# Kernel tuning notes

Hardware: AMD Instinct MI355X
Metric: run time of the kernel (lower is better)

## Reference

```python
import jax, jax.numpy as jnp
import numpy as np

B, S, IN = 1, 50000, 128
N = B * S
E = 800000
HID, HEADS, OUT = 64, 2, 64
NEG_SLOPE = 0.2
BN_EPS = 1e-5


def setup_inputs() -> dict:
    key = jax.random.key(0)
    ks = jax.random.split(key, 12)
    s = 0.1
    return {
        "data": jax.random.normal(ks[0], (B, S, IN), jnp.float32),
        "edge_index": jax.random.randint(ks[1], (2, E), 0, N, dtype=jnp.int64),
        "W0": jax.random.normal(ks[2], (IN, HEADS * HID), jnp.float32) * s,
        "att_src0": jax.random.normal(ks[3], (HEADS, HID), jnp.float32) * s,
        "att_dst0": jax.random.normal(ks[4], (HEADS, HID), jnp.float32) * s,
        "bias0": jnp.zeros((HEADS * HID,), jnp.float32),
        "gamma0": jnp.ones((HEADS * HID,), jnp.float32),
        "beta0": jnp.zeros((HEADS * HID,), jnp.float32),
        "W1": jax.random.normal(ks[5], (HEADS * HID, OUT), jnp.float32) * s,
        "att_src1": jax.random.normal(ks[6], (1, OUT), jnp.float32) * s,
        "att_dst1": jax.random.normal(ks[7], (1, OUT), jnp.float32) * s,
        "bias1": jnp.zeros((OUT,), jnp.float32),
    }


def gat_conv(x, edge_index, W, att_src, att_dst, bias, heads, ch, concat):
    n = x.shape[0]
    loop = jnp.arange(n, dtype=edge_index.dtype)
    src = jnp.concatenate([edge_index[0], loop])  # PyG adds self-loops by default
    dst = jnp.concatenate([edge_index[1], loop])
    h = (x @ W).reshape(n, heads, ch)  # [N,H,C]
    a_src = (h * att_src).sum(-1)  # [N,H]
    a_dst = (h * att_dst).sum(-1)  # [N,H]
    e = jax.nn.leaky_relu(a_src[src] + a_dst[dst], NEG_SLOPE)  # [Etot,H]
    m = jax.ops.segment_max(e, dst, num_segments=n)  # segment softmax over dst
    ex = jnp.exp(e - m[dst])
    denom = jax.ops.segment_sum(ex, dst, num_segments=n)
    alpha = ex / (denom[dst] + 1e-16)  # [Etot,H]
    out = jax.ops.segment_sum(h[src] * alpha[:, :, None], dst, num_segments=n)  # [N,H,C]
    out = out.reshape(n, heads * ch) if concat else out.mean(axis=1)
    return out + bias


def reference(data, edge_index, W0, att_src0, att_dst0, bias0, gamma0, beta0,
              W1, att_src1, att_dst1, bias1):
    x = data.reshape(N, IN)
    x = gat_conv(x, edge_index, W0, att_src0, att_dst0, bias0, HEADS, HID, True)
    mu = x.mean(axis=0)
    var = x.var(axis=0)
    x = (x - mu) * jax.lax.rsqrt(var + BN_EPS) * gamma0 + beta0  # BatchNorm1d (batch stats)
    x = jax.nn.elu(x)
    x = gat_conv(x, edge_index, W1, att_src1, att_dst1, bias1, 1, OUT, False)
    return x.reshape(B, S, OUT)
```

## Files before the change

kernel.cpp:

```cpp
#include <hip/hip_runtime.h>
#include <hip/hip_fp16.h>
#include <math.h>

#define N_NODES 50000
#define E_EDGES 800000
#define NEG_SLOPE 0.2f
#define BN_EPS 1e-5f
#define SCAN_NBLK ((N_NODES + 1023) / 1024)

__device__ __forceinline__ float lrelu(float v) { return v > 0.f ? v : NEG_SLOPE * v; }

__global__ void k_zero(int* __restrict__ counts, float* __restrict__ bn_sum,
                       float* __restrict__ bn_sumsq) {
  int i = blockIdx.x * 256 + threadIdx.x;
  if (i < N_NODES + 1) counts[i] = 0;
  if (i < 128) { bn_sum[i] = 0.f; bn_sumsq[i] = 0.f; }
}

__global__ void k_hist(const int* __restrict__ dst, int* __restrict__ counts) {
  int e = blockIdx.x * 256 + threadIdx.x;
  if (e < E_EDGES) atomicAdd(&counts[dst[e]], 1);
}

__global__ __launch_bounds__(256) void k_scan1(const int* __restrict__ counts,
                                               int* __restrict__ tmp_scan,
                                               int* __restrict__ blk_sums) {
  __shared__ int ts[256];
  int t = threadIdx.x;
  int base = blockIdx.x * 1024 + t * 4;
  int c0 = (base + 0 < N_NODES) ? counts[base + 0] : 0;
  int c1 = (base + 1 < N_NODES) ? counts[base + 1] : 0;
  int c2 = (base + 2 < N_NODES) ? counts[base + 2] : 0;
  int c3 = (base + 3 < N_NODES) ? counts[base + 3] : 0;
  int s = c0 + c1 + c2 + c3;
  ts[t] = s;
  __syncthreads();
  for (int off = 1; off < 256; off <<= 1) {
    int v = (t >= off) ? ts[t - off] : 0;
    __syncthreads();
    ts[t] += v;
    __syncthreads();
  }
  int excl = ts[t] - s;
  if (t == 255) blk_sums[blockIdx.x] = ts[255];
  if (base + 0 < N_NODES) tmp_scan[base + 0] = excl;
  if (base + 1 < N_NODES) tmp_scan[base + 1] = excl + c0;
  if (base + 2 < N_NODES) tmp_scan[base + 2] = excl + c0 + c1;
  if (base + 3 < N_NODES) tmp_scan[base + 3] = excl + c0 + c1 + c2;
}

__global__ void k_scan2(int* __restrict__ blk_sums) {
  int t = threadIdx.x;
  int orig = (t < SCAN_NBLK) ? blk_sums[t] : 0;
  int v = orig;
#pragma unroll
  for (int off = 1; off < 64; off <<= 1) {
    int u = __shfl_up(v, off);
    if (t >= off) v += u;
  }
  if (t < SCAN_NBLK) blk_sums[t] = v - orig;
}

__global__ __launch_bounds__(256) void k_scan3(const int* __restrict__ tmp_scan,
                                               const int* __restrict__ blk_sums,
                                               int* __restrict__ row_ptr,
                                               int* __restrict__ cursor) {
  int i = blockIdx.x * 256 + threadIdx.x;
  if (i < N_NODES) {
    int v = tmp_scan[i] + blk_sums[i >> 10];
    row_ptr[i] = v;
    cursor[i] = v;
  }
  if (i == 0) row_ptr[N_NODES] = E_EDGES;
}

__global__ void k_scatter(const int* __restrict__ src, const int* __restrict__ dst,
                          int* __restrict__ cursor, int* __restrict__ csr_src) {
  int e = blockIdx.x * 256 + threadIdx.x;
  if (e < E_EDGES) {
    int d = dst[e];
    int pos = atomicAdd(&cursor[d], 1);
    csr_src[pos] = src[e];
  }
}

__global__ __launch_bounds__(256) void k_gemm0(
    const float* __restrict__ x, const float* __restrict__ W,
    const float* __restrict__ att_s, const float* __restrict__ att_d,
    __half* __restrict__ h, float* __restrict__ a_src, float* __restrict__ a_dst) {
  __shared__ float xs[64 * 132];
  int t = threadIdx.x;
  int rowBase = blockIdx.x * 64;
#pragma unroll
  for (int j = 0; j < 8; j++) {
    int id = t + 256 * j;
    int row = id >> 5;
    int kk = (id & 31) * 4;
    float4 v = make_float4(0.f, 0.f, 0.f, 0.f);
    int gr = rowBase + row;
    if (gr < N_NODES) v = *(const float4*)&x[(size_t)gr * 128 + kk];
    *(float4*)&xs[row * 132 + kk] = v;
  }
  __syncthreads();

  int tc = t & 31, tr = t >> 5;
  int c = tc * 4, r0 = tr * 8;
  float acc[8][4];
#pragma unroll
  for (int i = 0; i < 8; i++)
#pragma unroll
    for (int j = 0; j < 4; j++) acc[i][j] = 0.f;

  for (int k4 = 0; k4 < 128; k4 += 4) {
    float4 wv[4];
#pragma unroll
    for (int kk = 0; kk < 4; kk++) wv[kk] = *(const float4*)&W[(k4 + kk) * 128 + c];
    float4 xv[8];
#pragma unroll
    for (int i = 0; i < 8; i++) xv[i] = *(const float4*)&xs[(r0 + i) * 132 + k4];
#pragma unroll
    for (int i = 0; i < 8; i++) {
      acc[i][0] += xv[i].x * wv[0].x + xv[i].y * wv[1].x + xv[i].z * wv[2].x + xv[i].w * wv[3].x;
      acc[i][1] += xv[i].x * wv[0].y + xv[i].y * wv[1].y + xv[i].z * wv[2].y + xv[i].w * wv[3].y;
      acc[i][2] += xv[i].x * wv[0].z + xv[i].y * wv[1].z + xv[i].z * wv[2].z + xv[i].w * wv[3].z;
      acc[i][3] += xv[i].x * wv[0].w + xv[i].y * wv[1].w + xv[i].z * wv[2].w + xv[i].w * wv[3].w;
    }
  }

  float as4[4], ad4[4];
#pragma unroll
  for (int j = 0; j < 4; j++) { as4[j] = att_s[c + j]; ad4[j] = att_d[c + j]; }
  int head = tc >> 4;
#pragma unroll
  for (int i = 0; i < 8; i++) {
    int gr = rowBase + r0 + i;
    float ps = acc[i][0] * as4[0] + acc[i][1] * as4[1] + acc[i][2] * as4[2] + acc[i][3] * as4[3];
    float pd = acc[i][0] * ad4[0] + acc[i][1] * ad4[1] + acc[i][2] * ad4[2] + acc[i][3] * ad4[3];
#pragma unroll
    for (int msk = 1; msk <= 8; msk <<= 1) {
      ps += __shfl_xor(ps, msk);
      pd += __shfl_xor(pd, msk);
    }
    if (gr < N_NODES) {
      __half2 p01 = __floats2half2_rn(acc[i][0], acc[i][1]);
      __half2 p23 = __floats2half2_rn(acc[i][2], acc[i][3]);
      uint2 pk;
      pk.x = *(unsigned int*)&p01;
      pk.y = *(unsigned int*)&p23;
      *(uint2*)&h[(size_t)gr * 128 + c] = pk;
      if ((t & 15) == 0) {
        a_src[gr * 2 + head] = ps;
        a_dst[gr * 2 + head] = pd;
      }
    }
  }
}

__global__ __launch_bounds__(256) void k_agg0(
    const int* __restrict__ row_ptr, const int* __restrict__ csr_src,
    const __half* __restrict__ h, const float* __restrict__ a_src,
    const float* __restrict__ a_dst, const float* __restrict__ bias,
    float* __restrict__ out) {
  int node = (blockIdx.x * blockDim.x + threadIdx.x) >> 6;
  if (node >= N_NODES) return;
  int l = threadIdx.x & 63;
  int head = l >> 5;
  int c = l * 2;
  float ad = a_dst[node * 2 + head];
  float m = lrelu(a_src[node * 2 + head] + ad);
  float d = 1.f;
  __half2 hvp = *(const __half2*)&h[(size_t)node * 128 + c];
  float2 hv = __half22float2(hvp);
  float acc0 = hv.x, acc1 = hv.y;
  int beg = row_ptr[node], end = row_ptr[node + 1];
  int i = beg;
  for (; i + 4 <= end; i += 4) {
    int s0 = csr_src[i], s1 = csr_src[i + 1], s2 = csr_src[i + 2], s3 = csr_src[i + 3];
    float e0 = lrelu(a_src[s0 * 2 + head] + ad);
    float e1 = lrelu(a_src[s1 * 2 + head] + ad);
    float e2 = lrelu(a_src[s2 * 2 + head] + ad);
    float e3 = lrelu(a_src[s3 * 2 + head] + ad);
    __half2 p0 = *(const __half2*)&h[(size_t)s0 * 128 + c];
    __half2 p1 = *(const __half2*)&h[(size_t)s1 * 128 + c];
    __half2 p2 = *(const __half2*)&h[(size_t)s2 * 128 + c];
    __half2 p3 = *(const __half2*)&h[(size_t)s3 * 128 + c];
    float nm = fmaxf(fmaxf(m, e0), fmaxf(fmaxf(e1, e2), e3));
    float sc = __expf(m - nm);
    float w0 = __expf(e0 - nm), w1 = __expf(e1 - nm);
    float w2 = __expf(e2 - nm), w3 = __expf(e3 - nm);
    d = d * sc + (w0 + w1) + (w2 + w3);
    float2 f0 = __half22float2(p0), f1 = __half22float2(p1);
    float2 f2 = __half22float2(p2), f3 = __half22float2(p3);
    acc0 = acc0 * sc + w0 * f0.x + w1 * f1.x + w2 * f2.x + w3 * f3.x;
    acc1 = acc1 * sc + w0 * f0.y + w1 * f1.y + w2 * f2.y + w3 * f3.y;
    m = nm;
  }
  for (; i < end; i++) {
    int s = csr_src[i];
    float ee = lrelu(a_src[s * 2 + head] + ad);
    __half2 pp = *(const __half2*)&h[(size_t)s * 128 + c];
    float nm = fmaxf(m, ee);
    float sc = __expf(m - nm);
    float w = __expf(ee - nm);
    float2 ff = __half22float2(pp);
    d = d * sc + w;
    acc0 = acc0 * sc + w * ff.x;
    acc1 = acc1 * sc + w * ff.y;
    m = nm;
  }
  float inv = 1.f / d;
  float2 o;
  o.x = acc0 * inv + bias[c];
  o.y = acc1 * inv + bias[c + 1];
  *(float2*)&out[(size_t)node * 128 + c] = o;
}

__global__ __launch_bounds__(256) void k_bnstats(const float* __restrict__ x,
                                                 float* __restrict__ bn_sum,
                                                 float* __restrict__ bn_sumsq) {
  int f = threadIdx.x & 127;
  int half = threadIdx.x >> 7;
  float s = 0.f, s2 = 0.f;
  for (int r = blockIdx.x * 2 + half; r < N_NODES; r += gridDim.x * 2) {
    float v = x[(size_t)r * 128 + f];
    s += v;
    s2 += v * v;
  }
  __shared__ float ls[256], ls2[256];
  ls[threadIdx.x] = s;
  ls2[threadIdx.x] = s2;
  __syncthreads();
  if (half == 0) {
    atomicAdd(&bn_sum[f], s + ls[f + 128]);
    atomicAdd(&bn_sumsq[f], s2 + ls2[f + 128]);
  }
}

__global__ void k_bnfinal(const float* __restrict__ sum, const float* __restrict__ sumsq,
                          const float* __restrict__ gamma, const float* __restrict__ beta,
                          float* __restrict__ scale, float* __restrict__ shift) {
  int f = threadIdx.x;
  float mu = sum[f] / (float)N_NODES;
  float var = sumsq[f] / (float)N_NODES - mu * mu;
  float sc = gamma[f] * rsqrtf(var + BN_EPS);
  scale[f] = sc;
  shift[f] = beta[f] - mu * sc;
}

__global__ __launch_bounds__(256) void k_gemm1(
    const float* __restrict__ x, const float* __restrict__ W,
    const float* __restrict__ scale, const float* __restrict__ shift,
    const float* __restrict__ att_s, const float* __restrict__ att_d,
    __half* __restrict__ h, float* __restrict__ a_src, float* __restrict__ a_dst) {
  __shared__ float xs[64 * 132];
  int t = threadIdx.x;
  int rowBase = blockIdx.x * 64;
#pragma unroll
  for (int j = 0; j < 8; j++) {
    int id = t + 256 * j;
    int row = id >> 5;
    int kk = (id & 31) * 4;
    float4 v = make_float4(0.f, 0.f, 0.f, 0.f);
    int gr = rowBase + row;
    if (gr < N_NODES) {
      float4 raw = *(const float4*)&x[(size_t)gr * 128 + kk];
      float4 sc = *(const float4*)&scale[kk];
      float4 sh = *(const float4*)&shift[kk];
      v.x = raw.x * sc.x + sh.x;
      v.y = raw.y * sc.y + sh.y;
      v.z = raw.z * sc.z + sh.z;
      v.w = raw.w * sc.w + sh.w;
      v.x = v.x > 0.f ? v.x : __expf(v.x) - 1.f;
      v.y = v.y > 0.f ? v.y : __expf(v.y) - 1.f;
      v.z = v.z > 0.f ? v.z : __expf(v.z) - 1.f;
      v.w = v.w > 0.f ? v.w : __expf(v.w) - 1.f;
    }
    *(float4*)&xs[row * 132 + kk] = v;
  }
  __syncthreads();

  int tc = t & 15, tr = t >> 4;
  int c = tc * 4, r0 = tr * 4;
  float acc[4][4];
#pragma unroll
  for (int i = 0; i < 4; i++)
#pragma unroll
    for (int j = 0; j < 4; j++) acc[i][j] = 0.f;

  for (int k4 = 0; k4 < 128; k4 += 4) {
    float4 wv[4];
#pragma unroll
    for (int kk = 0; kk < 4; kk++) wv[kk] = *(const float4*)&W[(k4 + kk) * 64 + c];
    float4 xv[4];
#pragma unroll
    for (int i = 0; i < 4; i++) xv[i] = *(const float4*)&xs[(r0 + i) * 132 + k4];
#pragma unroll
    for (int i = 0; i < 4; i++) {
      acc[i][0] += xv[i].x * wv[0].x + xv[i].y * wv[1].x + xv[i].z * wv[2].x + xv[i].w * wv[3].x;
      acc[i][1] += xv[i].x * wv[0].y + xv[i].y * wv[1].y + xv[i].z * wv[2].y + xv[i].w * wv[3].y;
      acc[i][2] += xv[i].x * wv[0].z + xv[i].y * wv[1].z + xv[i].z * wv[2].z + xv[i].w * wv[3].z;
      acc[i][3] += xv[i].x * wv[0].w + xv[i].y * wv[1].w + xv[i].z * wv[2].w + xv[i].w * wv[3].w;
    }
  }

  float as4[4], ad4[4];
#pragma unroll
  for (int j = 0; j < 4; j++) { as4[j] = att_s[c + j]; ad4[j] = att_d[c + j]; }
#pragma unroll
  for (int i = 0; i < 4; i++) {
    int gr = rowBase + r0 + i;
    float ps = acc[i][0] * as4[0] + acc[i][1] * as4[1] + acc[i][2] * as4[2] + acc[i][3] * as4[3];
    float pd = acc[i][0] * ad4[0] + acc[i][1] * ad4[1] + acc[i][2] * ad4[2] + acc[i][3] * ad4[3];
#pragma unroll
    for (int msk = 1; msk <= 8; msk <<= 1) {
      ps += __shfl_xor(ps, msk);
      pd += __shfl_xor(pd, msk);
    }
    if (gr < N_NODES) {
      __half2 p01 = __floats2half2_rn(acc[i][0], acc[i][1]);
      __half2 p23 = __floats2half2_rn(acc[i][2], acc[i][3]);
      uint2 pk;
      pk.x = *(unsigned int*)&p01;
      pk.y = *(unsigned int*)&p23;
      *(uint2*)&h[(size_t)gr * 64 + c] = pk;
      if ((t & 15) == 0) {
        a_src[gr] = ps;
        a_dst[gr] = pd;
      }
    }
  }
}

__global__ __launch_bounds__(256) void k_agg1(
    const int* __restrict__ row_ptr, const int* __restrict__ csr_src,
    const __half* __restrict__ h, const float* __restrict__ a_src,
    const float* __restrict__ a_dst, const float* __restrict__ bias,
    float* __restrict__ out) {
  int node = (blockIdx.x * blockDim.x + threadIdx.x) >> 6;
  if (node >= N_NODES) return;
  int l = threadIdx.x & 63;
  float ad = a_dst[node];
  float m = lrelu(a_src[node] + ad);
  float d = 1.f;
  float acc = __half2float(h[(size_t)node * 64 + l]);
  int beg = row_ptr[node], end = row_ptr[node + 1];
  int i = beg;
  for (; i + 4 <= end; i += 4) {
    int s0 = csr_src[i], s1 = csr_src[i + 1], s2 = csr_src[i + 2], s3 = csr_src[i + 3];
    float e0 = lrelu(a_src[s0] + ad);
    float e1 = lrelu(a_src[s1] + ad);
    float e2 = lrelu(a_src[s2] + ad);
    float e3 = lrelu(a_src[s3] + ad);
    __half p0 = h[(size_t)s0 * 64 + l];
    __half p1 = h[(size_t)s1 * 64 + l];
    __half p2 = h[(size_t)s2 * 64 + l];
    __half p3 = h[(size_t)s3 * 64 + l];
    float nm = fmaxf(fmaxf(m, e0), fmaxf(fmaxf(e1, e2), e3));
    float sc = __expf(m - nm);
    float w0 = __expf(e0 - nm), w1 = __expf(e1 - nm);
    float w2 = __expf(e2 - nm), w3 = __expf(e3 - nm);
    d = d * sc + (w0 + w1) + (w2 + w3);
    acc = acc * sc + w0 * __half2float(p0) + w1 * __half2float(p1) +
          w2 * __half2float(p2) + w3 * __half2float(p3);
    m = nm;
  }
  for (; i < end; i++) {
    int s = csr_src[i];
    float ee = lrelu(a_src[s] + ad);
    __half pp = h[(size_t)s * 64 + l];
    float nm = fmaxf(m, ee);
    float sc = __expf(m - nm);
    float w = __expf(ee - nm);
    d = d * sc + w;
    acc = acc * sc + w * __half2float(pp);
    m = nm;
  }
  out[(size_t)node * 64 + l] = acc / d + bias[l];
}

extern "C" void kernel_launch(void* const* d_in, const int* in_sizes, int n_in,
                              void* d_out, int out_size, void* d_ws, size_t ws_size,
                              hipStream_t stream) {
  const float* data = (const float*)d_in[0];
  const int* ei = (const int*)d_in[1];
  const float* W0 = (const float*)d_in[2];
  const float* att_src0 = (const float*)d_in[3];
  const float* att_dst0 = (const float*)d_in[4];
  const float* bias0 = (const float*)d_in[5];
  const float* gamma0 = (const float*)d_in[6];
  const float* beta0 = (const float*)d_in[7];
  const float* W1 = (const float*)d_in[8];
  const float* att_src1 = (const float*)d_in[9];
  const float* att_dst1 = (const float*)d_in[10];
  const float* bias1 = (const float*)d_in[11];
  float* out = (float*)d_out;

  char* ws = (char*)d_ws;
  size_t off = 0;
  auto alloc = [&](size_t bytes) -> void* {
    void* p = ws + off;
    off = (off + bytes + 255) & ~(size_t)255;
    return p;
  };
  int* row_ptr = (int*)alloc((N_NODES + 1) * 4);
  int* counts = (int*)alloc((N_NODES + 1) * 4);
  int* cursor = (int*)alloc(N_NODES * 4);
  int* tmp_scan = (int*)alloc((size_t)N_NODES * 4);
  int* blk_sums = (int*)alloc(64 * 4);
  int* csr_src = (int*)alloc((size_t)E_EDGES * 4);
  __half* h0 = (__half*)alloc((size_t)N_NODES * 128 * 2);
  float* a_s0 = (float*)alloc((size_t)N_NODES * 2 * 4);
  float* a_d0 = (float*)alloc((size_t)N_NODES * 2 * 4);
  float* out0 = (float*)alloc((size_t)N_NODES * 128 * 4);
  float* bn_sum = (float*)alloc(128 * 4);
  float* bn_sumsq = (float*)alloc(128 * 4);
  float* bn_scale = (float*)alloc(128 * 4);
  float* bn_shift = (float*)alloc(128 * 4);
  __half* h1 = h0;
  float* a_s1 = a_s0;
  float* a_d1 = a_d0;

  const int* srcArr = ei;
  const int* dstArr = ei + E_EDGES;

  k_zero<<<(N_NODES + 256) / 256, 256, 0, stream>>>(counts, bn_sum, bn_sumsq);
  k_hist<<<(E_EDGES + 255) / 256, 256, 0, stream>>>(dstArr, counts);
  k_scan1<<<SCAN_NBLK, 256, 0, stream>>>(counts, tmp_scan, blk_sums);
  k_scan2<<<1, 64, 0, stream>>>(blk_sums);
  k_scan3<<<(N_NODES + 255) / 256, 256, 0, stream>>>(tmp_scan, blk_sums, row_ptr, cursor);
  k_scatter<<<(E_EDGES + 255) / 256, 256, 0, stream>>>(srcArr, dstArr, cursor, csr_src);
  k_gemm0<<<(N_NODES + 63) / 64, 256, 0, stream>>>(data, W0, att_src0, att_dst0, h0, a_s0, a_d0);
  k_agg0<<<(N_NODES + 3) / 4, 256, 0, stream>>>(row_ptr, csr_src, h0, a_s0, a_d0, bias0, out0);
  k_bnstats<<<1024, 256, 0, stream>>>(out0, bn_sum, bn_sumsq);
  k_bnfinal<<<1, 128, 0, stream>>>(bn_sum, bn_sumsq, gamma0, beta0, bn_scale, bn_shift);
  k_gemm1<<<(N_NODES + 63) / 64, 256, 0, stream>>>(out0, W1, bn_scale, bn_shift, att_src1,
                                                   att_dst1, h1, a_s1, a_d1);
  k_agg1<<<(N_NODES + 3) / 4, 256, 0, stream>>>(row_ptr, csr_src, h1, a_s1, a_d1, bias1, out);
}
```

Measured before the change: 353.0 us.

## Bin edges by destination range before CSR scatter; unroll aggregation by eight

The single random-atomic CSR scatter is replaced by two passes. First, edges are staged in shared-memory bins of 2048 destination nodes and flushed as packed (src<<16|dst) words into per-bin regions. Then one 1024-thread block per bin scatters into csr_src, so its atomics and writes stay within a small address range. Both aggregation kernels also gain an 8-edge unrolled loop to keep more gathers in flight. The cost is an extra pass over the edges, many block barriers in the binning kernel, and only 25 blocks in the second scatter pass, which may leave the GPU underused.

```diff
diff --git a/kernel.cpp b/kernel.cpp
--- a/kernel.cpp
+++ b/kernel.cpp
@@ -7,6 +7,11 @@
 #define NEG_SLOPE 0.2f
 #define BN_EPS 1e-5f
 #define SCAN_NBLK ((N_NODES + 1023) / 1024)
+#define NB 25
+#define BIN_K 384
+#define BIN_FLUSH 128
+#define BIN_NBLK 256
+#define BIN_CHUNK ((E_EDGES + BIN_NBLK - 1) / BIN_NBLK)
 
 __device__ __forceinline__ float lrelu(float v) { return v > 0.f ? v : NEG_SLOPE * v; }
 
@@ -64,23 +69,83 @@
 __global__ __launch_bounds__(256) void k_scan3(const int* __restrict__ tmp_scan,
                                                const int* __restrict__ blk_sums,
                                                int* __restrict__ row_ptr,
-                                               int* __restrict__ cursor) {
+                                               int* __restrict__ cursor,
+                                               int* __restrict__ bin_cursor) {
   int i = blockIdx.x * 256 + threadIdx.x;
   if (i < N_NODES) {
     int v = tmp_scan[i] + blk_sums[i >> 10];
     row_ptr[i] = v;
     cursor[i] = v;
+    if ((i & 2047) == 0) bin_cursor[i >> 11] = v;
   }
   if (i == 0) row_ptr[N_NODES] = E_EDGES;
 }
 
-__global__ void k_scatter(const int* __restrict__ src, const int* __restrict__ dst,
-                          int* __restrict__ cursor, int* __restrict__ csr_src) {
-  int e = blockIdx.x * 256 + threadIdx.x;
-  if (e < E_EDGES) {
-    int d = dst[e];
+__global__ __launch_bounds__(256) void k_bin(const int* __restrict__ src,
+                                             const int* __restrict__ dst,
+                                             int* __restrict__ bin_cursor,
+                                             unsigned int* __restrict__ binned) {
+  __shared__ unsigned int bins[NB][BIN_K];
+  __shared__ int fill[NB];
+  __shared__ int flush_base[NB];
+  int t = threadIdx.x;
+  if (t < NB) fill[t] = 0;
+  __syncthreads();
+  int chunkBeg = blockIdx.x * BIN_CHUNK;
+  int chunkEnd = chunkBeg + BIN_CHUNK;
+  if (chunkEnd > E_EDGES) chunkEnd = E_EDGES;
+  for (int base = chunkBeg; base < chunkEnd; base += 256) {
+    int e = base + t;
+    if (e < chunkEnd) {
+      unsigned int d = (unsigned int)dst[e];
+      int b = d >> 11;
+      int pos = atomicAdd(&fill[b], 1);
+      bins[b][pos] = ((unsigned int)src[e] << 16) | d;
+    }
+    __syncthreads();
+    if (t < NB) {
+      int f = fill[t];
+      flush_base[t] = (f >= BIN_FLUSH) ? atomicAdd(&bin_cursor[t], f) : -1;
+    }
+    __syncthreads();
+    for (int b = 0; b < NB; b++) {
+      int fb = flush_base[b];
+      if (fb >= 0) {
+        int f = fill[b];
+        for (int k = t; k < f; k += 256) binned[fb + k] = bins[b][k];
+      }
+    }
+    __syncthreads();
+    if (t < NB && flush_base[t] >= 0) fill[t] = 0;
+    __syncthreads();
+  }
+  if (t < NB) {
+    int f = fill[t];
+    flush_base[t] = (f > 0) ? atomicAdd(&bin_cursor[t], f) : -1;
+  }
+  __syncthreads();
+  for (int b = 0; b < NB; b++) {
+    int fb = flush_base[b];
+    if (fb >= 0) {
+      int f = fill[b];
+      for (int k = t; k < f; k += 256) binned[fb + k] = bins[b][k];
+    }
+  }
+}
+
+__global__ __launch_bounds__(1024) void k_scatter2(const int* __restrict__ row_ptr,
+                                                   const unsigned int* __restrict__ binned,
+                                                   int* __restrict__ cursor,
+                                                   int* __restrict__ csr_src) {
+  int b = blockIdx.x;
+  int beg = row_ptr[b << 11];
+  int hi = (b + 1) << 11;
+  int end = row_ptr[hi < N_NODES ? hi : N_NODES];
+  for (int i = beg + threadIdx.x; i < end; i += 1024) {
+    unsigned int v = binned[i];
+    int d = (int)(v & 0xFFFFu);
     int pos = atomicAdd(&cursor[d], 1);
-    csr_src[pos] = src[e];
+    csr_src[pos] = (int)(v >> 16);
   }
 }
 
@@ -169,25 +234,52 @@
   float ad = a_dst[node * 2 + head];
   float m = lrelu(a_src[node * 2 + head] + ad);
   float d = 1.f;
-  __half2 hvp = *(const __half2*)&h[(size_t)node * 128 + c];
-  float2 hv = __half22float2(hvp);
+  float2 hv = __half22float2(*(const __half2*)&h[(size_t)node * 128 + c]);
   float acc0 = hv.x, acc1 = hv.y;
   int beg = row_ptr[node], end = row_ptr[node + 1];
   int i = beg;
+  for (; i + 8 <= end; i += 8) {
+    int s0 = csr_src[i], s1 = csr_src[i + 1], s2 = csr_src[i + 2], s3 = csr_src[i + 3];
+    int s4 = csr_src[i + 4], s5 = csr_src[i + 5], s6 = csr_src[i + 6], s7 = csr_src[i + 7];
+    float e0 = lrelu(a_src[s0 * 2 + head] + ad), e1 = lrelu(a_src[s1 * 2 + head] + ad);
+    float e2 = lrelu(a_src[s2 * 2 + head] + ad), e3 = lrelu(a_src[s3 * 2 + head] + ad);
+    float e4 = lrelu(a_src[s4 * 2 + head] + ad), e5 = lrelu(a_src[s5 * 2 + head] + ad);
+    float e6 = lrelu(a_src[s6 * 2 + head] + ad), e7 = lrelu(a_src[s7 * 2 + head] + ad);
+    __half2 p0 = *(const __half2*)&h[(size_t)s0 * 128 + c];
+    __half2 p1 = *(const __half2*)&h[(size_t)s1 * 128 + c];
+    __half2 p2 = *(const __half2*)&h[(size_t)s2 * 128 + c];
+    __half2 p3 = *(const __half2*)&h[(size_t)s3 * 128 + c];
+    __half2 p4 = *(const __half2*)&h[(size_t)s4 * 128 + c];
+    __half2 p5 = *(const __half2*)&h[(size_t)s5 * 128 + c];
+    __half2 p6 = *(const __half2*)&h[(size_t)s6 * 128 + c];
+    __half2 p7 = *(const __half2*)&h[(size_t)s7 * 128 + c];
+    float nm = fmaxf(m, fmaxf(fmaxf(fmaxf(e0, e1), fmaxf(e2, e3)),
+                              fmaxf(fmaxf(e4, e5), fmaxf(e6, e7))));
+    float sc = __expf(m - nm);
+    float w0 = __expf(e0 - nm), w1 = __expf(e1 - nm), w2 = __expf(e2 - nm), w3 = __expf(e3 - nm);
+    float w4 = __expf(e4 - nm), w5 = __expf(e5 - nm), w6 = __expf(e6 - nm), w7 = __expf(e7 - nm);
+    d = d * sc + ((w0 + w1) + (w2 + w3)) + ((w4 + w5) + (w6 + w7));
+    float2 f0 = __half22float2(p0), f1 = __half22float2(p1);
+    float2 f2 = __half22float2(p2), f3 = __half22float2(p3);
+    float2 f4 = __half22float2(p4), f5 = __half22float2(p5);
+    float2 f6 = __half22float2(p6), f7 = __half22float2(p7);
+    acc0 = acc0 * sc + (w0 * f0.x + w1 * f1.x + w2 * f2.x + w3 * f3.x) +
+           (w4 * f4.x + w5 * f5.x + w6 * f6.x + w7 * f7.x);
+    acc1 = acc1 * sc + (w0 * f0.y + w1 * f1.y + w2 * f2.y + w3 * f3.y) +
+           (w4 * f4.y + w5 * f5.y + w6 * f6.y + w7 * f7.y);
+    m = nm;
+  }
   for (; i + 4 <= end; i += 4) {
     int s0 = csr_src[i], s1 = csr_src[i + 1], s2 = csr_src[i + 2], s3 = csr_src[i + 3];
-    float e0 = lrelu(a_src[s0 * 2 + head] + ad);
-    float e1 = lrelu(a_src[s1 * 2 + head] + ad);
-    float e2 = lrelu(a_src[s2 * 2 + head] + ad);
-    float e3 = lrelu(a_src[s3 * 2 + head] + ad);
+    float e0 = lrelu(a_src[s0 * 2 + head] + ad), e1 = lrelu(a_src[s1 * 2 + head] + ad);
+    float e2 = lrelu(a_src[s2 * 2 + head] + ad), e3 = lrelu(a_src[s3 * 2 + head] + ad);
     __half2 p0 = *(const __half2*)&h[(size_t)s0 * 128 + c];
     __half2 p1 = *(const __half2*)&h[(size_t)s1 * 128 + c];
     __half2 p2 = *(const __half2*)&h[(size_t)s2 * 128 + c];
     __half2 p3 = *(const __half2*)&h[(size_t)s3 * 128 + c];
     float nm = fmaxf(fmaxf(m, e0), fmaxf(fmaxf(e1, e2), e3));
     float sc = __expf(m - nm);
-    float w0 = __expf(e0 - nm), w1 = __expf(e1 - nm);
-    float w2 = __expf(e2 - nm), w3 = __expf(e3 - nm);
+    float w0 = __expf(e0 - nm), w1 = __expf(e1 - nm), w2 = __expf(e2 - nm), w3 = __expf(e3 - nm);
     d = d * sc + (w0 + w1) + (w2 + w3);
     float2 f0 = __half22float2(p0), f1 = __half22float2(p1);
     float2 f2 = __half22float2(p2), f3 = __half22float2(p3);
@@ -345,23 +437,42 @@
   float acc = __half2float(h[(size_t)node * 64 + l]);
   int beg = row_ptr[node], end = row_ptr[node + 1];
   int i = beg;
+  for (; i + 8 <= end; i += 8) {
+    int s0 = csr_src[i], s1 = csr_src[i + 1], s2 = csr_src[i + 2], s3 = csr_src[i + 3];
+    int s4 = csr_src[i + 4], s5 = csr_src[i + 5], s6 = csr_src[i + 6], s7 = csr_src[i + 7];
+    float e0 = lrelu(a_src[s0] + ad), e1 = lrelu(a_src[s1] + ad);
+    float e2 = lrelu(a_src[s2] + ad), e3 = lrelu(a_src[s3] + ad);
+    float e4 = lrelu(a_src[s4] + ad), e5 = lrelu(a_src[s5] + ad);
+    float e6 = lrelu(a_src[s6] + ad), e7 = lrelu(a_src[s7] + ad);
+    __half p0 = h[(size_t)s0 * 64 + l], p1 = h[(size_t)s1 * 64 + l];
+    __half p2 = h[(size_t)s2 * 64 + l], p3 = h[(size_t)s3 * 64 + l];
+    __half p4 = h[(size_t)s4 * 64 + l], p5 = h[(size_t)s5 * 64 + l];
+    __half p6 = h[(size_t)s6 * 64 + l], p7 = h[(size_t)s7 * 64 + l];
+    float nm = fmaxf(m, fmaxf(fmaxf(fmaxf(e0, e1), fmaxf(e2, e3)),
+                              fmaxf(fmaxf(e4, e5), fmaxf(e6, e7))));
+    float sc = __expf(m - nm);
+    float w0 = __expf(e0 - nm), w1 = __expf(e1 - nm), w2 = __expf(e2 - nm), w3 = __expf(e3 - nm);
+    float w4 = __expf(e4 - nm), w5 = __expf(e5 - nm), w6 = __expf(e6 - nm), w7 = __expf(e7 - nm);
+    d = d * sc + ((w0 + w1) + (w2 + w3)) + ((w4 + w5) + (w6 + w7));
+    acc = acc * sc +
+          (w0 * __half2float(p0) + w1 * __half2float(p1) + w2 * __half2float(p2) +
+           w3 * __half2float(p3)) +
+          (w4 * __half2float(p4) + w5 * __half2float(p5) + w6 * __half2float(p6) +
+           w7 * __half2float(p7));
+    m = nm;
+  }
   for (; i + 4 <= end; i += 4) {
     int s0 = csr_src[i], s1 = csr_src[i + 1], s2 = csr_src[i + 2], s3 = csr_src[i + 3];
-    float e0 = lrelu(a_src[s0] + ad);
-    float e1 = lrelu(a_src[s1] + ad);
-    float e2 = lrelu(a_src[s2] + ad);
-    float e3 = lrelu(a_src[s3] + ad);
-    __half p0 = h[(size_t)s0 * 64 + l];
-    __half p1 = h[(size_t)s1 * 64 + l];
-    __half p2 = h[(size_t)s2 * 64 + l];
-    __half p3 = h[(size_t)s3 * 64 + l];
+    float e0 = lrelu(a_src[s0] + ad), e1 = lrelu(a_src[s1] + ad);
+    float e2 = lrelu(a_src[s2] + ad), e3 = lrelu(a_src[s3] + ad);
+    __half p0 = h[(size_t)s0 * 64 + l], p1 = h[(size_t)s1 * 64 + l];
+    __half p2 = h[(size_t)s2 * 64 + l], p3 = h[(size_t)s3 * 64 + l];
     float nm = fmaxf(fmaxf(m, e0), fmaxf(fmaxf(e1, e2), e3));
     float sc = __expf(m - nm);
-    float w0 = __expf(e0 - nm), w1 = __expf(e1 - nm);
-    float w2 = __expf(e2 - nm), w3 = __expf(e3 - nm);
+    float w0 = __expf(e0 - nm), w1 = __expf(e1 - nm), w2 = __expf(e2 - nm), w3 = __expf(e3 - nm);
     d = d * sc + (w0 + w1) + (w2 + w3);
-    acc = acc * sc + w0 * __half2float(p0) + w1 * __half2float(p1) +
-          w2 * __half2float(p2) + w3 * __half2float(p3);
+    acc = acc * sc + w0 * __half2float(p0) + w1 * __half2float(p1) + w2 * __half2float(p2) +
+          w3 * __half2float(p3);
     m = nm;
   }
   for (; i < end; i++) {
@@ -407,6 +518,8 @@
   int* cursor = (int*)alloc(N_NODES * 4);
   int* tmp_scan = (int*)alloc((size_t)N_NODES * 4);
   int* blk_sums = (int*)alloc(64 * 4);
+  int* bin_cursor = (int*)alloc(NB * 4);
+  unsigned int* binned = (unsigned int*)alloc((size_t)E_EDGES * 4);
   int* csr_src = (int*)alloc((size_t)E_EDGES * 4);
   __half* h0 = (__half*)alloc((size_t)N_NODES * 128 * 2);
   float* a_s0 = (float*)alloc((size_t)N_NODES * 2 * 4);
@@ -427,8 +540,10 @@
   k_hist<<<(E_EDGES + 255) / 256, 256, 0, stream>>>(dstArr, counts);
   k_scan1<<<SCAN_NBLK, 256, 0, stream>>>(counts, tmp_scan, blk_sums);
   k_scan2<<<1, 64, 0, stream>>>(blk_sums);
-  k_scan3<<<(N_NODES + 255) / 256, 256, 0, stream>>>(tmp_scan, blk_sums, row_ptr, cursor);
-  k_scatter<<<(E_EDGES + 255) / 256, 256, 0, stream>>>(srcArr, dstArr, cursor, csr_src);
+  k_scan3<<<(N_NODES + 255) / 256, 256, 0, stream>>>(tmp_scan, blk_sums, row_ptr, cursor,
+                                                     bin_cursor);
+  k_bin<<<BIN_NBLK, 256, 0, stream>>>(srcArr, dstArr, bin_cursor, binned);
+  k_scatter2<<<NB, 1024, 0, stream>>>(row_ptr, binned, cursor, csr_src);
   k_gemm0<<<(N_NODES + 63) / 64, 256, 0, stream>>>(data, W0, att_src0, att_dst0, h0, a_s0, a_d0);
   k_agg0<<<(N_NODES + 3) / 4, 256, 0, stream>>>(row_ptr, csr_src, h0, a_s0, a_d0, bias0, out0);
   k_bnstats<<<1024, 256, 0, stream>>>(out0, bn_sum, bn_sumsq);
```

Result: slower. 423.4 us (+20.0%).
